# Kernel optimization log

Measured on AMD Instinct MI355X. Metric: run time of the kernel, lower is better.

## Reference

```python
import jax, jax.numpy as jnp
import numpy as np

N_HEAD = 16

def setup_inputs() -> dict:
    key = jax.random.key(0)
    k1, k2, k3, k4, k5 = jax.random.split(key, 5)
    B, T, C = 8, 2048, 1024
    hs = C // N_HEAD  # 64
    return {
        "ids": jax.random.normal(k1, (B, T, C), dtype=jnp.float32),
        "qkv_w": jax.random.normal(k2, (3 * hs, C), dtype=jnp.float32) * (C ** -0.5),
        "qkv_b": jax.random.normal(k3, (3 * hs,), dtype=jnp.float32) * 0.02,
        "proj_w": jax.random.normal(k4, (C, C), dtype=jnp.float32) * (C ** -0.5),
        "proj_b": jax.random.normal(k5, (C,), dtype=jnp.float32) * 0.02,
    }

def reference(ids, qkv_w, qkv_b, proj_w, proj_b):
    B, T, C = ids.shape
    hs = qkv_w.shape[0] // 3  # head_size
    # All heads share the same qkv Linear (input is replicated per-head in the
    # original), so compute one head and tile at the end.
    qkv = ids @ qkv_w.T + qkv_b                      # [B,T,3*hs]
    q, k, v = jnp.split(qkv, 3, axis=-1)             # each [B,T,hs]
    wei = jnp.einsum('btd,bsd->bts', q, k)           # [B,T,T]
    tril = jnp.tril(jnp.ones((T, T), dtype=bool))
    wei = jnp.where(tril, wei, jnp.float32(0.0))     # causal mask (no softmax)
    out_h = jnp.einsum('bts,bsd->btd', wei, v)       # [B,T,hs]
    out = jnp.tile(out_h, (1, 1, N_HEAD))            # identical heads concatenated
    return out @ proj_w.T + proj_b                   # [B,T,C]
```

## Files before the change

### kernel.cpp

```cpp
#include <hip/hip_runtime.h>
#include <hip/hip_bf16.h>

#define Bsz 8
#define Tsz 2048
#define Csz 1024
#define HSsz 64
#define NQ 192

typedef __attribute__((ext_vector_type(8))) short short8v;
typedef __attribute__((ext_vector_type(4))) float f32x4;
typedef unsigned short ushortT;
typedef unsigned int uintT;

__device__ __forceinline__ unsigned int f2bf(float f) {
    union { float f; unsigned int u; } v; v.f = f;
    return (v.u + 0x7fffu + ((v.u >> 16) & 1u)) >> 16;
}

__device__ __forceinline__ unsigned int pk2bf(float lo, float hi) {
    union { __hip_bfloat162 h2; unsigned int u; } cv;
    cv.h2 = __float22bfloat162_rn(float2{lo, hi});
    return cv.u;
}

__global__ __launch_bounds__(256) void k_prep(const float* __restrict__ qw,
                                              const float* __restrict__ pw,
                                              ushortT* __restrict__ wB,
                                              ushortT* __restrict__ w2a) {
    const int blk = blockIdx.x;
    if (blk < 96) {
        int idx = blk * 256 + threadIdx.x;
        int l = idx & 63;
        int ksjt = idx >> 6;
        int jt = ksjt % 12, ks = ksjt / 12;
        int j = jt * 16 + (l & 15);
        int k = ks * 32 + (l >> 4) * 8;
        const float* src = &qw[j * Csz + k];
        float4 a = *(const float4*)src;
        float4 b = *(const float4*)(src + 4);
        uint4 o;
        o.x = f2bf(a.x) | (f2bf(a.y) << 16);
        o.y = f2bf(a.z) | (f2bf(a.w) << 16);
        o.z = f2bf(b.x) | (f2bf(b.y) << 16);
        o.w = f2bf(b.z) | (f2bf(b.w) << 16);
        *(uint4*)&wB[(size_t)idx * 8] = o;
    } else {
        int idx = (blk - 96) * 256 + threadIdx.x;
        int l = idx & 63;
        int rest = idx >> 6;
        int m = rest & 63, ks = rest >> 6;
        int c = m * 16 + (l & 15);
        int d0 = ks * 32 + (l >> 4) * 8;
        float s0 = 0, s1 = 0, s2 = 0, s3 = 0, s4 = 0, s5 = 0, s6 = 0, s7 = 0;
#pragma unroll
        for (int hh = 0; hh < 16; ++hh) {
            const float* p = &pw[c * Csz + hh * HSsz + d0];
            float4 x = *(const float4*)p;
            float4 y = *(const float4*)(p + 4);
            s0 += x.x; s1 += x.y; s2 += x.z; s3 += x.w;
            s4 += y.x; s5 += y.y; s6 += y.z; s7 += y.w;
        }
        uint4 o;
        o.x = f2bf(s0) | (f2bf(s1) << 16);
        o.y = f2bf(s2) | (f2bf(s3) << 16);
        o.z = f2bf(s4) | (f2bf(s5) << 16);
        o.w = f2bf(s6) | (f2bf(s7) << 16);
        *(uint4*)&w2a[(size_t)idx * 8] = o;
    }
}

__global__ __launch_bounds__(512, 4) void k_qkv_mfma(const float* __restrict__ ids,
                                                     const ushortT* __restrict__ wB,
                                                     const float* __restrict__ bias,
                                                     ushortT* __restrict__ Qf,
                                                     ushortT* __restrict__ Kf,
                                                     ushortT* __restrict__ Vf) {
    __shared__ float sA[2][32 * 132];
    uintT* Lqk = (uintT*)&sA[0][0];
    uintT* Lv  = Lqk + 32 * 68;

    const int tid = threadIdx.x;
    const int wv  = tid >> 6;
    const int l   = tid & 63;
    const int wm  = wv >> 2;
    const int wn  = wv & 3;
    const int lg  = l >> 4, ll = l & 15;

    const int row0 = blockIdx.x * 32;

    const int srow = tid >> 4;
    const int scol = (tid & 15) * 8;
    const float* gsrc = ids + (size_t)(row0 + srow) * Csz + scol;

    const int afrow = wm * 16 + ll;

    f32x4 acc[3];
    acc[0] = acc[1] = acc[2] = (f32x4){0.f, 0.f, 0.f, 0.f};

    float4 st0 = *(const float4*)gsrc;
    float4 st1 = *(const float4*)(gsrc + 4);

    const ushortT* bbase_p = wB + ((size_t)(wn * 3) * 64 + l) * 8;

    for (int c = 0; c < 8; ++c) {
        float* bufp = &sA[c & 1][0];
        float* wp = &bufp[srow * 132 + scol];
        *(float4*)wp = st0;
        *(float4*)(wp + 4) = st1;
        __syncthreads();
        if (c < 7) {
            st0 = *(const float4*)(gsrc + (c + 1) * 128);
            st1 = *(const float4*)(gsrc + (c + 1) * 128 + 4);
        }
#pragma unroll
        for (int kk = 0; kk < 4; ++kk) {
            const ushortT* bp = bbase_p + (size_t)(4 * c + kk) * 6144;
            short8v b0 = *(const short8v*)(bp);
            short8v b1 = *(const short8v*)(bp + 512);
            short8v b2 = *(const short8v*)(bp + 1024);

            const float* ap = &bufp[afrow * 132 + kk * 32 + lg * 8];
            float4 a0 = *(const float4*)ap;
            float4 a1 = *(const float4*)(ap + 4);
            union { short8v s; unsigned int u[4]; } af;
            af.u[0] = pk2bf(a0.x, a0.y); af.u[1] = pk2bf(a0.z, a0.w);
            af.u[2] = pk2bf(a1.x, a1.y); af.u[3] = pk2bf(a1.z, a1.w);

            acc[0] = __builtin_amdgcn_mfma_f32_16x16x32_bf16(af.s, b0, acc[0], 0, 0, 0);
            acc[1] = __builtin_amdgcn_mfma_f32_16x16x32_bf16(af.s, b1, acc[1], 0, 0, 0);
            acc[2] = __builtin_amdgcn_mfma_f32_16x16x32_bf16(af.s, b2, acc[2], 0, 0, 0);
        }
    }
    __syncthreads();

    const int crow_l = wm * 16 + lg * 4;
    ushortT* L16 = (ushortT*)Lqk;
#pragma unroll
    for (int n = 0; n < 3; ++n) {
        const int jb = wn * 3 + n;
        const int j  = jb * 16 + ll;
        const float bj = bias[j];
        float v0 = acc[n][0] + bj, v1 = acc[n][1] + bj;
        float v2 = acc[n][2] + bj, v3 = acc[n][3] + bj;
        if (jb < 8) {
            ushortT* p = &L16[crow_l * 136 + j];
            p[0]   = (ushortT)f2bf(v0);
            p[136] = (ushortT)f2bf(v1);
            p[272] = (ushortT)f2bf(v2);
            p[408] = (ushortT)f2bf(v3);
        } else {
            uintT* p = &Lv[(j - 128) * 20 + (crow_l >> 1)];
            p[0] = pk2bf(v0, v1);
            p[1] = pk2bf(v2, v3);
        }
    }
    __syncthreads();

    const int l2 = tid & 63, ll2 = l2 & 15, lg2 = l2 >> 4;
    if (tid < 256) {
        const int ks = (tid >> 6) & 1, m = tid >> 7;
        uint4 q = *(const uint4*)&Lqk[(m * 16 + ll2) * 68 + ks * 16 + lg2 * 4];
        *(uint4*)&Qf[(((size_t)(row0 >> 4) + m) * 2 + ks) * 512 + l2 * 8] = q;
        const int n = tid >> 6;
        uint4 v = *(const uint4*)&Lv[(n * 16 + ll2) * 20 + lg2 * 4];
        const int bb = row0 >> 11, s32 = (row0 >> 5) & 63;
        *(uint4*)&Vf[((((size_t)bb * 64 + s32) * 4 + n) * 64 + l2) * 8] = v;
    } else {
        const int ks = (tid >> 6) & 1, m = (tid >> 7) & 1;
        uint4 k = *(const uint4*)&Lqk[(m * 16 + ll2) * 68 + 32 + ks * 16 + lg2 * 4];
        *(uint4*)&Kf[(((size_t)(row0 >> 4) + m) * 2 + ks) * 512 + l2 * 8] = k;
    }
}

__global__ __launch_bounds__(256, 3) void k_attn_proj(const ushortT* __restrict__ Qf,
                                                      const ushortT* __restrict__ Kf,
                                                      const ushortT* __restrict__ Vf,
                                                      const ushortT* __restrict__ w2a,
                                                      const float* __restrict__ pb,
                                                      float* __restrict__ out) {
    __shared__ uintT su[4 * 2 * 16 * 36];
    __shared__ float s_o[4][32 * 68];

    const int tid = threadIdx.x;
    const int w  = tid >> 6;
    const int l  = tid & 63;
    const int lg = l >> 4;
    const int ll = l & 15;

    const int u = blockIdx.x;
    const int b = u / 48;
    const int r = u - b * 48;

    int si, sub, nsub;
    const bool heavy = (r < 32);
    if (heavy) { si = 63 - r; sub = w; nsub = 4; }
    else {
        const int rr = r - 32;
        si = (w < 2) ? (31 - rr) : rr;
        sub = w & 1; nsub = 2;
    }
    const int nT  = (si >> 1) + 1;
    const int qn  = nT / nsub, rem = nT % nsub;
    const int t0  = sub * qn + (sub < rem ? sub : rem);
    const int cnt = qn + (sub < rem ? 1 : 0);

    const int gq = b * 128 + si * 2;

    short8v qf[2][2];
#pragma unroll
    for (int mt = 0; mt < 2; ++mt)
#pragma unroll
        for (int ks = 0; ks < 2; ++ks)
            qf[mt][ks] = *(const short8v*)&Qf[(((size_t)gq + mt) * 2 + ks) * 512 + l * 8];

    f32x4 oacc[2][4];
#pragma unroll
    for (int mt = 0; mt < 2; ++mt)
#pragma unroll
        for (int n = 0; n < 4; ++n) oacc[mt][n] = (f32x4){0.f, 0.f, 0.f, 0.f};

    for (int tile = t0; tile < t0 + cnt; ++tile) {
        const int gs = b * 128 + tile * 4;
        short8v kf[4][2];
#pragma unroll
        for (int ms = 0; ms < 4; ++ms) {
            const ushortT* kp = &Kf[(((size_t)gs + ms) * 2) * 512 + l * 8];
            kf[ms][0] = *(const short8v*)kp;
            kf[ms][1] = *(const short8v*)(kp + 512);
        }
        f32x4 sacc[4][2];
#pragma unroll
        for (int ms = 0; ms < 4; ++ms)
#pragma unroll
            for (int mt = 0; mt < 2; ++mt) sacc[ms][mt] = (f32x4){0.f, 0.f, 0.f, 0.f};
#pragma unroll
        for (int ms = 0; ms < 4; ++ms)
#pragma unroll
            for (int mt = 0; mt < 2; ++mt) {
                sacc[ms][mt] = __builtin_amdgcn_mfma_f32_16x16x32_bf16(kf[ms][0], qf[mt][0], sacc[ms][mt], 0, 0, 0);
                sacc[ms][mt] = __builtin_amdgcn_mfma_f32_16x16x32_bf16(kf[ms][1], qf[mt][1], sacc[ms][mt], 0, 0, 0);
            }
        if (tile == nT - 1) {
#pragma unroll
            for (int ms = 0; ms < 4; ++ms)
#pragma unroll
                for (int mt = 0; mt < 2; ++mt) {
                    const int tg = si * 32 + mt * 16 + ll;
#pragma unroll
                    for (int rr2 = 0; rr2 < 4; ++rr2) {
                        int sg = tile * 64 + ms * 16 + 4 * lg + rr2;
                        if (sg > tg) sacc[ms][mt][rr2] = 0.f;
                    }
                }
        }
#pragma unroll
        for (int mt = 0; mt < 2; ++mt)
#pragma unroll
            for (int ms = 0; ms < 4; ++ms) {
                uint2 pk;
                pk.x = pk2bf(sacc[ms][mt][0], sacc[ms][mt][1]);
                pk.y = pk2bf(sacc[ms][mt][2], sacc[ms][mt][3]);
                *(uint2*)&su[((w * 2 + mt) * 16 + ll) * 36 + ms * 8 + 2 * lg] = pk;
            }
        union { uint4 u4; short8v s; } pa[2][2];
#pragma unroll
        for (int mt = 0; mt < 2; ++mt)
#pragma unroll
            for (int h = 0; h < 2; ++h)
                pa[mt][h].u4 = *(const uint4*)&su[((w * 2 + mt) * 16 + ll) * 36 + h * 16 + lg * 4];

        const int gv = b * 64 + tile * 2;
        short8v vf[2][4];
#pragma unroll
        for (int h = 0; h < 2; ++h)
#pragma unroll
            for (int n = 0; n < 4; ++n)
                vf[h][n] = *(const short8v*)&Vf[((((size_t)gv + h) * 4 + n) * 64 + l) * 8];
#pragma unroll
        for (int mt = 0; mt < 2; ++mt)
#pragma unroll
            for (int n = 0; n < 4; ++n) {
                oacc[mt][n] = __builtin_amdgcn_mfma_f32_16x16x32_bf16(pa[mt][0].s, vf[0][n], oacc[mt][n], 0, 0, 0);
                oacc[mt][n] = __builtin_amdgcn_mfma_f32_16x16x32_bf16(pa[mt][1].s, vf[1][n], oacc[mt][n], 0, 0, 0);
            }
    }

#pragma unroll
    for (int mt = 0; mt < 2; ++mt)
#pragma unroll
        for (int n = 0; n < 4; ++n)
#pragma unroll
            for (int rr2 = 0; rr2 < 4; ++rr2)
                s_o[w][(mt * 16 + 4 * lg + rr2) * 68 + 16 * n + ll] = oacc[mt][n][rr2];
    __syncthreads();

    int pstrip, nsum, wb0, mstart, mcount;
    if (heavy) { pstrip = si; nsum = 4; wb0 = 0; mstart = w * 16; mcount = 16; }
    else {
        const int rr = r - 32;
        pstrip = (w < 2) ? (31 - rr) : rr;
        nsum = 2; wb0 = (w < 2) ? 0 : 2;
        mstart = (w & 1) * 32; mcount = 32;
    }

    union { short8v s; unsigned int u[4]; } hbf[2][2];
#pragma unroll
    for (int mt = 0; mt < 2; ++mt)
#pragma unroll
        for (int ks = 0; ks < 2; ++ks) {
            float4 A = {0.f, 0.f, 0.f, 0.f}, B2 = {0.f, 0.f, 0.f, 0.f};
            for (int w2 = wb0; w2 < wb0 + nsum; ++w2) {
                const float* p = &s_o[w2][(mt * 16 + ll) * 68 + ks * 32 + lg * 8];
                const float4 x = *(const float4*)p;
                const float4 y = *(const float4*)(p + 4);
                A.x += x.x; A.y += x.y; A.z += x.z; A.w += x.w;
                B2.x += y.x; B2.y += y.y; B2.z += y.z; B2.w += y.w;
            }
            hbf[mt][ks].u[0] = pk2bf(A.x, A.y);
            hbf[mt][ks].u[1] = pk2bf(A.z, A.w);
            hbf[mt][ks].u[2] = pk2bf(B2.x, B2.y);
            hbf[mt][ks].u[3] = pk2bf(B2.z, B2.w);
        }

    const int gt = b * Tsz + pstrip * 32;
    const int crow = lg * 4;
#pragma unroll 4
    for (int m = mstart; m < mstart + mcount; ++m) {
        const ushortT* ap = w2a + (size_t)(m * 64 + l) * 8;
        short8v a0 = *(const short8v*)ap;
        short8v a1 = *(const short8v*)(ap + 32768);
        const float4 pv = *(const float4*)&pb[m * 16 + crow];
#pragma unroll
        for (int mt = 0; mt < 2; ++mt) {
            f32x4 acc = (f32x4){0.f, 0.f, 0.f, 0.f};
            acc = __builtin_amdgcn_mfma_f32_16x16x32_bf16(a0, hbf[mt][0].s, acc, 0, 0, 0);
            acc = __builtin_amdgcn_mfma_f32_16x16x32_bf16(a1, hbf[mt][1].s, acc, 0, 0, 0);
            float4 o;
            o.x = acc[0] + pv.x; o.y = acc[1] + pv.y;
            o.z = acc[2] + pv.z; o.w = acc[3] + pv.w;
            *(float4*)&out[(size_t)(gt + mt * 16 + ll) * Csz + m * 16 + crow] = o;
        }
    }
}

extern "C" void kernel_launch(void* const* d_in, const int* in_sizes, int n_in,
                              void* d_out, int out_size, void* d_ws, size_t ws_size,
                              hipStream_t stream) {
    const float* ids    = (const float*)d_in[0];
    const float* qkv_w  = (const float*)d_in[1];
    const float* qkv_b  = (const float*)d_in[2];
    const float* proj_w = (const float*)d_in[3];
    const float* proj_b = (const float*)d_in[4];
    float* out = (float*)d_out;

    ushortT* Qf  = (ushortT*)d_ws;
    ushortT* Kf  = Qf + 16384 * HSsz;
    ushortT* Vf  = Kf + 16384 * HSsz;
    ushortT* wB  = Vf + 16384 * HSsz;
    ushortT* w2a = wB + 196608;

    hipLaunchKernelGGL(k_prep,      dim3(128), dim3(256), 0, stream, qkv_w, proj_w, wB, w2a);
    hipLaunchKernelGGL(k_qkv_mfma,  dim3(512), dim3(512), 0, stream, ids, wB, qkv_b, Qf, Kf, Vf);
    hipLaunchKernelGGL(k_attn_proj, dim3(384), dim3(256), 0, stream, Qf, Kf, Vf, w2a, proj_b, out);
}
```

Measured before the change: 72.83 us.

## Use one 8-wave block per query strip with split-K tiles

Restructures the attention+projection kernel so each 512-thread block handles a single 32-row query strip, with key tiles split across 8 waves. This replaces the heavy/light strip-pairing scheme with 4-wave blocks. The blocks are ordered so the longest strips are scheduled first, and LDS is shared between the P staging buffer and the partial-sum reduction, which is now done per 16-row half. MFMA sections are also wrapped in s_setprio to favour matrix issue. The cost is more partial sums to reduce and extra barriers, and short strips leave many waves idle.

```diff
diff --git a/kernel.cpp b/kernel.cpp
--- a/kernel.cpp
+++ b/kernel.cpp
@@ -172,14 +172,15 @@
     }
 }
 
-__global__ __launch_bounds__(256, 3) void k_attn_proj(const ushortT* __restrict__ Qf,
+__global__ __launch_bounds__(512, 4) void k_attn_proj(const ushortT* __restrict__ Qf,
                                                       const ushortT* __restrict__ Kf,
                                                       const ushortT* __restrict__ Vf,
                                                       const ushortT* __restrict__ w2a,
                                                       const float* __restrict__ pb,
                                                       float* __restrict__ out) {
-    __shared__ uintT su[4 * 2 * 16 * 36];
-    __shared__ float s_o[4][32 * 68];
+    __shared__ uintT lds_raw[16 * 16 * 36];
+    uintT* su = lds_raw;
+    float* s_o = (float*)lds_raw;
 
     const int tid = threadIdx.x;
     const int w  = tid >> 6;
@@ -188,21 +189,13 @@
     const int ll = l & 15;
 
     const int u = blockIdx.x;
-    const int b = u / 48;
-    const int r = u - b * 48;
-
-    int si, sub, nsub;
-    const bool heavy = (r < 32);
-    if (heavy) { si = 63 - r; sub = w; nsub = 4; }
-    else {
-        const int rr = r - 32;
-        si = (w < 2) ? (31 - rr) : rr;
-        sub = w & 1; nsub = 2;
-    }
+    const int b = u & 7;
+    const int si = 63 - (u >> 3);
+
     const int nT  = (si >> 1) + 1;
-    const int qn  = nT / nsub, rem = nT % nsub;
-    const int t0  = sub * qn + (sub < rem ? sub : rem);
-    const int cnt = qn + (sub < rem ? 1 : 0);
+    const int qn  = nT >> 3, rem = nT & 7;
+    const int t0  = w * qn + (w < rem ? w : rem);
+    const int cnt = qn + (w < rem ? 1 : 0);
 
     const int gq = b * 128 + si * 2;
 
@@ -233,6 +226,7 @@
         for (int ms = 0; ms < 4; ++ms)
 #pragma unroll
             for (int mt = 0; mt < 2; ++mt) sacc[ms][mt] = (f32x4){0.f, 0.f, 0.f, 0.f};
+        __builtin_amdgcn_s_setprio(1);
 #pragma unroll
         for (int ms = 0; ms < 4; ++ms)
 #pragma unroll
@@ -240,6 +234,7 @@
                 sacc[ms][mt] = __builtin_amdgcn_mfma_f32_16x16x32_bf16(kf[ms][0], qf[mt][0], sacc[ms][mt], 0, 0, 0);
                 sacc[ms][mt] = __builtin_amdgcn_mfma_f32_16x16x32_bf16(kf[ms][1], qf[mt][1], sacc[ms][mt], 0, 0, 0);
             }
+        __builtin_amdgcn_s_setprio(0);
         if (tile == nT - 1) {
 #pragma unroll
             for (int ms = 0; ms < 4; ++ms)
@@ -276,6 +271,7 @@
 #pragma unroll
             for (int n = 0; n < 4; ++n)
                 vf[h][n] = *(const short8v*)&Vf[((((size_t)gv + h) * 4 + n) * 64 + l) * 8];
+        __builtin_amdgcn_s_setprio(1);
 #pragma unroll
         for (int mt = 0; mt < 2; ++mt)
 #pragma unroll
@@ -283,62 +279,53 @@
                 oacc[mt][n] = __builtin_amdgcn_mfma_f32_16x16x32_bf16(pa[mt][0].s, vf[0][n], oacc[mt][n], 0, 0, 0);
                 oacc[mt][n] = __builtin_amdgcn_mfma_f32_16x16x32_bf16(pa[mt][1].s, vf[1][n], oacc[mt][n], 0, 0, 0);
             }
-    }
-
-#pragma unroll
-    for (int mt = 0; mt < 2; ++mt)
+        __builtin_amdgcn_s_setprio(0);
+    }
+
+    const int gt = b * Tsz + si * 32;
+#pragma unroll
+    for (int mt = 0; mt < 2; ++mt) {
+        __syncthreads();
 #pragma unroll
         for (int n = 0; n < 4; ++n)
 #pragma unroll
             for (int rr2 = 0; rr2 < 4; ++rr2)
-                s_o[w][(mt * 16 + 4 * lg + rr2) * 68 + 16 * n + ll] = oacc[mt][n][rr2];
-    __syncthreads();
-
-    int pstrip, nsum, wb0, mstart, mcount;
-    if (heavy) { pstrip = si; nsum = 4; wb0 = 0; mstart = w * 16; mcount = 16; }
-    else {
-        const int rr = r - 32;
-        pstrip = (w < 2) ? (31 - rr) : rr;
-        nsum = 2; wb0 = (w < 2) ? 0 : 2;
-        mstart = (w & 1) * 32; mcount = 32;
-    }
-
-    union { short8v s; unsigned int u[4]; } hbf[2][2];
-#pragma unroll
-    for (int mt = 0; mt < 2; ++mt)
+                s_o[w * 1088 + (4 * lg + rr2) * 68 + 16 * n + ll] = oacc[mt][n][rr2];
+        __syncthreads();
+
+        union { short8v s; uintT uu[4]; } hbf[2];
 #pragma unroll
         for (int ks = 0; ks < 2; ++ks) {
             float4 A = {0.f, 0.f, 0.f, 0.f}, B2 = {0.f, 0.f, 0.f, 0.f};
-            for (int w2 = wb0; w2 < wb0 + nsum; ++w2) {
-                const float* p = &s_o[w2][(mt * 16 + ll) * 68 + ks * 32 + lg * 8];
+#pragma unroll
+            for (int w2 = 0; w2 < 8; ++w2) {
+                const float* p = &s_o[w2 * 1088 + ll * 68 + ks * 32 + lg * 8];
                 const float4 x = *(const float4*)p;
                 const float4 y = *(const float4*)(p + 4);
                 A.x += x.x; A.y += x.y; A.z += x.z; A.w += x.w;
                 B2.x += y.x; B2.y += y.y; B2.z += y.z; B2.w += y.w;
             }
-            hbf[mt][ks].u[0] = pk2bf(A.x, A.y);
-            hbf[mt][ks].u[1] = pk2bf(A.z, A.w);
-            hbf[mt][ks].u[2] = pk2bf(B2.x, B2.y);
-            hbf[mt][ks].u[3] = pk2bf(B2.z, B2.w);
-        }
-
-    const int gt = b * Tsz + pstrip * 32;
-    const int crow = lg * 4;
-#pragma unroll 4
-    for (int m = mstart; m < mstart + mcount; ++m) {
-        const ushortT* ap = w2a + (size_t)(m * 64 + l) * 8;
-        short8v a0 = *(const short8v*)ap;
-        short8v a1 = *(const short8v*)(ap + 32768);
-        const float4 pv = *(const float4*)&pb[m * 16 + crow];
-#pragma unroll
-        for (int mt = 0; mt < 2; ++mt) {
+            hbf[ks].uu[0] = pk2bf(A.x, A.y);
+            hbf[ks].uu[1] = pk2bf(A.z, A.w);
+            hbf[ks].uu[2] = pk2bf(B2.x, B2.y);
+            hbf[ks].uu[3] = pk2bf(B2.z, B2.w);
+        }
+
+        const size_t orow = (size_t)(gt + mt * 16 + ll) * Csz;
+#pragma unroll
+        for (int m = w * 8; m < w * 8 + 8; ++m) {
+            const ushortT* ap = w2a + (size_t)(m * 64 + l) * 8;
+            short8v a0 = *(const short8v*)ap;
+            short8v a1 = *(const short8v*)(ap + 32768);
             f32x4 acc = (f32x4){0.f, 0.f, 0.f, 0.f};
-            acc = __builtin_amdgcn_mfma_f32_16x16x32_bf16(a0, hbf[mt][0].s, acc, 0, 0, 0);
-            acc = __builtin_amdgcn_mfma_f32_16x16x32_bf16(a1, hbf[mt][1].s, acc, 0, 0, 0);
+            acc = __builtin_amdgcn_mfma_f32_16x16x32_bf16(a0, hbf[0].s, acc, 0, 0, 0);
+            acc = __builtin_amdgcn_mfma_f32_16x16x32_bf16(a1, hbf[1].s, acc, 0, 0, 0);
+            const int c0 = m * 16 + lg * 4;
+            const float4 pv = *(const float4*)&pb[c0];
             float4 o;
             o.x = acc[0] + pv.x; o.y = acc[1] + pv.y;
             o.z = acc[2] + pv.z; o.w = acc[3] + pv.w;
-            *(float4*)&out[(size_t)(gt + mt * 16 + ll) * Csz + m * 16 + crow] = o;
+            *(float4*)&out[orow + c0] = o;
         }
     }
 }
@@ -361,5 +348,5 @@
 
     hipLaunchKernelGGL(k_prep,      dim3(128), dim3(256), 0, stream, qkv_w, proj_w, wB, w2a);
     hipLaunchKernelGGL(k_qkv_mfma,  dim3(512), dim3(512), 0, stream, ids, wB, qkv_b, Qf, Kf, Vf);
-    hipLaunchKernelGGL(k_attn_proj, dim3(384), dim3(256), 0, stream, Qf, Kf, Vf, w2a, proj_b, out);
-}
+    hipLaunchKernelGGL(k_attn_proj, dim3(512), dim3(512), 0, stream, Qf, Kf, Vf, w2a, proj_b, out);
+}
```

Result: faster. 59.75 us (-18.0%).
